# Kernel tuning notes

Measured on AMD Instinct MI355X. Metric: run time of the kernel, lower is better.

## Reference

```python
import jax, jax.numpy as jnp
import numpy as np

QMAX = 127.0          # int8 clip bound (symmetric, preserve-zero)
QDIV = 127.5          # AQT int8 scale divisor: 2**(bits-1) - 0.5


def _safe(s):
    # avoid div-by-zero for all-zero rows/cols
    return jnp.where(s == 0.0, 1.0, s)


def setup_inputs() -> dict:
    key = jax.random.key(0)
    k1, k2 = jax.random.split(key)
    lhs = jax.random.normal(k1, (8192, 4096), dtype=jnp.float32)
    rhs = jax.random.normal(k2, (4096, 4096), dtype=jnp.float32)
    return {"lhs": lhs, "rhs": rhs}


def reference(lhs, rhs):
    # --- dynamic symmetric int8 quantization (AQT abs-max calibration) ---
    # lhs: contract over axis 1 -> per-row scale [M, 1]
    s_l = _safe(jnp.max(jnp.abs(lhs), axis=1, keepdims=True) / QDIV)
    # rhs: contract over axis 0 -> per-column scale [1, N]
    s_r = _safe(jnp.max(jnp.abs(rhs), axis=0, keepdims=True) / QDIV)

    q_l = jnp.clip(jnp.round(lhs / s_l), -QMAX, QMAX).astype(jnp.int8)
    q_r = jnp.clip(jnp.round(rhs / s_r), -QMAX, QMAX).astype(jnp.int8)

    # --- integer matmul with int32 accumulation ---
    acc = jax.lax.dot_general(
        q_l, q_r,
        dimension_numbers=(((1,), (0,)), ((), ())),
        preferred_element_type=jnp.int32,
    )

    # --- dequantize: outer product of per-row / per-column scales ---
    return acc.astype(jnp.float32) * s_l * s_r
```

## Files before the change

kernel.cpp:

```cpp
#include <hip/hip_runtime.h>
#include <stdint.h>

#define M_DIM 8192
#define N_DIM 4096
#define K_DIM 4096
#define QMAXF 127.0f
#define QDIVF 127.5f

typedef int v4i __attribute__((ext_vector_type(4)));

typedef __attribute__((address_space(3))) void lds_void_t;
typedef __attribute__((address_space(1))) const void glb_void_t;

static __device__ __forceinline__ void load_lds16(const void* g, void* l) {
    __builtin_amdgcn_global_load_lds((glb_void_t*)g, (lds_void_t*)l, 16, 0, 0);
}

__global__ __launch_bounds__(256) void prep1_kernel(
        const float* __restrict__ lhs, const float* __restrict__ rhs,
        float* __restrict__ sL, unsigned* __restrict__ bits,
        int8_t* __restrict__ ql) {
    const int t = threadIdx.x;
    if (blockIdx.x < M_DIM) {
        const int row = blockIdx.x;
        const float4* rp = (const float4*)(lhs + (size_t)row * K_DIM);
        float4 v[4];
        float m = 0.0f;
#pragma unroll
        for (int i = 0; i < 4; ++i) {
            v[i] = rp[t + i * 256];
            m = fmaxf(m, fmaxf(fmaxf(fabsf(v[i].x), fabsf(v[i].y)),
                               fmaxf(fabsf(v[i].z), fabsf(v[i].w))));
        }
#pragma unroll
        for (int off = 32; off; off >>= 1) m = fmaxf(m, __shfl_down(m, off, 64));
        __shared__ float wmax[4];
        if ((t & 63) == 0) wmax[t >> 6] = m;
        __syncthreads();
        const float mm = fmaxf(fmaxf(wmax[0], wmax[1]), fmaxf(wmax[2], wmax[3]));
        float s = mm / QDIVF;
        s = (s == 0.0f) ? 1.0f : s;
        if (t == 0) sL[row] = s;
        unsigned* qo = (unsigned*)ql + (size_t)row * 1024;
#pragma unroll
        for (int i = 0; i < 4; ++i) {
            int q0 = (int)fminf(fmaxf(rintf(v[i].x / s), -QMAXF), QMAXF);
            int q1 = (int)fminf(fmaxf(rintf(v[i].y / s), -QMAXF), QMAXF);
            int q2 = (int)fminf(fmaxf(rintf(v[i].z / s), -QMAXF), QMAXF);
            int q3 = (int)fminf(fmaxf(rintf(v[i].w / s), -QMAXF), QMAXF);
            qo[t + i * 256] = (q0 & 255) | ((q1 & 255) << 8) | ((q2 & 255) << 16)
                            | ((unsigned)(q3 & 255) << 24);
        }
    } else {
        const int cb = blockIdx.x - M_DIM;
        const int col = (cb & 15) * 256 + t;
        const int r0 = (cb >> 4) * 64;
        float m = 0.0f;
#pragma unroll 4
        for (int r = 0; r < 64; ++r)
            m = fmaxf(m, fabsf(rhs[(size_t)(r0 + r) * N_DIM + col]));
        atomicMax(&bits[col], __float_as_uint(m));
    }
}

__global__ __launch_bounds__(256) void quant_rhs_t_kernel(
        const float* __restrict__ rhs, const unsigned* __restrict__ bits,
        float* __restrict__ sR, int8_t* __restrict__ qbT) {
    __shared__ __align__(16) int8_t lt[64][80];
    const int n0 = blockIdx.x * 64;
    const int k0 = blockIdx.y * 64;
    const int t = threadIdx.x;
    const int nloc = t & 63;
    const int kq = (t >> 6) * 16;
    float s = __uint_as_float(bits[n0 + nloc]) / QDIVF;
    s = (s == 0.0f) ? 1.0f : s;
    if (blockIdx.y == 0 && t < 64) {
        float ss = __uint_as_float(bits[n0 + t]) / QDIVF;
        sR[n0 + t] = (ss == 0.0f) ? 1.0f : ss;
    }
#pragma unroll
    for (int i = 0; i < 4; ++i) {
        unsigned pack = 0;
#pragma unroll
        for (int j = 0; j < 4; ++j) {
            int kk = kq + i * 4 + j;
            float x = rhs[(size_t)(k0 + kk) * N_DIM + n0 + nloc];
            int q = (int)fminf(fmaxf(rintf(x / s), -QMAXF), QMAXF);
            pack |= (unsigned)(q & 255) << (8 * j);
        }
        *(unsigned*)&lt[nloc][kq + i * 4] = pack;
    }
    __syncthreads();
    const int nn = t >> 2, ch = t & 3;
    v4i val = *(const v4i*)&lt[nn][ch * 16];
    *(v4i*)&qbT[(size_t)(n0 + nn) * K_DIM + k0 + ch * 16] = val;
}


#define BAR() do { asm volatile("" ::: "memory");          \
                   __builtin_amdgcn_s_barrier();           \
                   asm volatile("" ::: "memory"); } while (0)

#define VMCNT(N) asm volatile("s_waitcnt vmcnt(%0)" :: "n"(N) : "memory")

#define TILE(KT, BUF, PAR, SA, SB, VM) do {                                     \
    if (SA) {                                                                   \
        _Pragma("unroll") for (int mm = 0; mm < 4; ++mm)                        \
            an[(PAR) ^ 1][mm] = *(const v4i*)(pa[mm] + ((KT) + 1) * 64);        \
    }                                                                           \
    if (SB) {                                                                   \
        load_lds16(gB0 + (size_t)((KT) + 2) * 64,                               \
                   lds + (((KT) + 2) & 3) * 16384 + sdst);                      \
        load_lds16(gB0 + (size_t)128 * K_DIM + (size_t)((KT) + 2) * 64,         \
                   lds + (((KT) + 2) & 3) * 16384 + 8192 + sdst);               \
    }                                                                           \
    _Pragma("unroll") for (int nn = 0; nn < 8; ++nn)                            \
        bf[nn] = *(const v4i*)(lds + (BUF) * 16384 + boff[nn]);                 \
    __builtin_amdgcn_s_setprio(1);                                              \
    _Pragma("unroll") for (int mm = 0; mm < 4; ++mm)                            \
    _Pragma("unroll") for (int nn = 0; nn < 8; ++nn)                            \
        acc[mm][nn] = __builtin_amdgcn_mfma_i32_16x16x64_i8(                    \
            an[PAR][mm], bf[nn], acc[mm][nn], 0, 0, 0);                         \
    __builtin_amdgcn_s_setprio(0);                                              \
    VMCNT(VM);                                                                  \
    BAR();                                                                      \
} while (0)

__global__ __launch_bounds__(512, 2) void gemm_i8_kernel(
        const int8_t* __restrict__ qa, const int8_t* __restrict__ qbT,
        const float* __restrict__ sL, const float* __restrict__ sR,
        float* __restrict__ out) {
    __shared__ __align__(16) int8_t lds[65536];

    const int t = threadIdx.x;
    const int wave = t >> 6;
    const int lane = t & 63;

    const int bid = blockIdx.x;
    const int xcd = bid & 7;
    const int idx = bid >> 3;
    const int mt = (xcd >> 1) * 8 + (idx >> 3);
    const int nt = (xcd & 1) * 8 + (idx & 7);
    const int brow = mt * 256;
    const int bcol = nt * 256;

    const int wm = (wave >> 1) * 64;
    const int wn = (wave & 1) * 128;

    const int8_t* pa[4];
#pragma unroll
    for (int m = 0; m < 4; ++m)
        pa[m] = qa + (size_t)(brow + wm + m * 16 + (lane & 15)) * K_DIM
                   + (lane >> 4) * 16;

    int boff[8];
#pragma unroll
    for (int n = 0; n < 8; ++n) {
        int row = wn + n * 16 + (lane & 15);
        boff[n] = row * 64 + (((lane >> 4) ^ ((row >> 1) & 3)) * 16);
    }

    v4i acc[4][8];
#pragma unroll
    for (int m = 0; m < 4; ++m)
#pragma unroll
        for (int n = 0; n < 8; ++n) acc[m][n] = (v4i){0, 0, 0, 0};

    const int srow = t >> 2;
    const int lcA = (t & 3) ^ ((srow >> 1) & 3);
    const int8_t* gB0 = qbT + (size_t)(bcol + srow) * K_DIM + lcA * 16;
    const int sdst = t * 16;

    v4i an[2][4], bf[8];

    load_lds16(gB0,                             lds + sdst);
    load_lds16(gB0 + (size_t)128 * K_DIM,       lds + 8192 + sdst);
    load_lds16(gB0 + 64,                        lds + 16384 + sdst);
    load_lds16(gB0 + (size_t)128 * K_DIM + 64,  lds + 16384 + 8192 + sdst);
#pragma unroll
    for (int mm = 0; mm < 4; ++mm) an[0][mm] = *(const v4i*)(pa[mm]);
    VMCNT(6);
    BAR();

    for (int kt = 0; kt < 60; kt += 4) {
        TILE(kt + 0, 0, 0, 1, 1, 6);
        TILE(kt + 1, 1, 1, 1, 1, 6);
        TILE(kt + 2, 2, 0, 1, 1, 6);
        TILE(kt + 3, 3, 1, 1, 1, 6);
    }
    TILE(60, 0, 0, 1, 1, 6);
    TILE(61, 1, 1, 1, 1, 6);
    TILE(62, 2, 0, 1, 0, 4);
    TILE(63, 3, 1, 0, 0, 0);

    const int r4 = (lane >> 4) * 4;
    const int cc = lane & 15;
#pragma unroll
    for (int m = 0; m < 4; ++m) {
        const int grow0 = brow + wm + m * 16 + r4;
        const float s0 = sL[grow0 + 0];
        const float s1 = sL[grow0 + 1];
        const float s2 = sL[grow0 + 2];
        const float s3 = sL[grow0 + 3];
#pragma unroll
        for (int n = 0; n < 8; ++n) {
            const int gcol = bcol + wn + n * 16 + cc;
            const float sc = sR[gcol];
            float* o = out + (size_t)grow0 * N_DIM + gcol;
            o[0 * N_DIM] = (float)acc[m][n][0] * s0 * sc;
            o[1 * N_DIM] = (float)acc[m][n][1] * s1 * sc;
            o[2 * N_DIM] = (float)acc[m][n][2] * s2 * sc;
            o[3 * N_DIM] = (float)acc[m][n][3] * s3 * sc;
        }
    }
}

extern "C" void kernel_launch(void* const* d_in, const int* in_sizes, int n_in,
                              void* d_out, int out_size, void* d_ws, size_t ws_size,
                              hipStream_t stream) {
    const float* lhs = (const float*)d_in[0];
    const float* rhs = (const float*)d_in[1];
    float* out = (float*)d_out;

    uint8_t* ws = (uint8_t*)d_ws;
    int8_t* ql    = (int8_t*)ws;
    int8_t* qbT   = (int8_t*)(ws + 33554432);
    float* sL     = (float*)(ws + 50331648);
    float* sR     = (float*)(ws + 50331648 + 32768);
    unsigned* bits = (unsigned*)(ws + 50331648 + 32768 + 16384);

    hipMemsetAsync(bits, 0, N_DIM * sizeof(unsigned), stream);

    prep1_kernel<<<M_DIM + 1024, 256, 0, stream>>>(lhs, rhs, sL, bits, ql);
    quant_rhs_t_kernel<<<dim3(N_DIM / 64, K_DIM / 64), 256, 0, stream>>>(
        rhs, bits, sR, qbT);
    gemm_i8_kernel<<<dim3((M_DIM / 256) * (N_DIM / 256)), 512, 0, stream>>>(
        ql, qbT, sL, sR, out);
}
```

Before: 263.1 us.

## Stage A tiles through LDS with 4-deep pipeline and 128x128 per-wave tiles

```diff
diff --git a/kernel.cpp b/kernel.cpp
--- a/kernel.cpp
+++ b/kernel.cpp
@@ -103,34 +103,39 @@
 
 #define VMCNT(N) asm volatile("s_waitcnt vmcnt(%0)" :: "n"(N) : "memory")
 
-#define TILE(KT, BUF, PAR, SA, SB, VM) do {                                     \
-    if (SA) {                                                                   \
-        _Pragma("unroll") for (int mm = 0; mm < 4; ++mm)                        \
-            an[(PAR) ^ 1][mm] = *(const v4i*)(pa[mm] + ((KT) + 1) * 64);        \
+#define STAGE_ALL(KT, BQ) do {                                                  \
+    _Pragma("unroll") for (int h = 0; h < 4; ++h)                               \
+        load_lds16(gA0 + (size_t)(h * 64) * K_DIM + (size_t)(KT) * 64,          \
+                   lds + (BQ) * 32768 + h * 4096 + sdst);                       \
+    _Pragma("unroll") for (int h = 0; h < 4; ++h)                               \
+        load_lds16(gB0 + (size_t)(h * 64) * K_DIM + (size_t)(KT) * 64,          \
+                   lds + (BQ) * 32768 + 16384 + h * 4096 + sdst);               \
+} while (0)
+
+#define TILE(KT, P, RDN, S, VM, DOBAR) do {                                     \
+    if (DOBAR) { VMCNT(VM); BAR(); }                                            \
+    if (RDN) {                                                                  \
+        _Pragma("unroll") for (int mm = 0; mm < 8; ++mm)                        \
+            af[(P) ^ 1][mm] = *(const v4i*)(                                    \
+                lds + (((KT) + 1) & 3) * 32768 + aoff[mm]);                     \
+        _Pragma("unroll") for (int nn = 0; nn < 8; ++nn)                        \
+            bf[(P) ^ 1][nn] = *(const v4i*)(                                    \
+                lds + (((KT) + 1) & 3) * 32768 + boff[nn]);                     \
     }                                                                           \
-    if (SB) {                                                                   \
-        load_lds16(gB0 + (size_t)((KT) + 2) * 64,                               \
-                   lds + (((KT) + 2) & 3) * 16384 + sdst);                      \
-        load_lds16(gB0 + (size_t)128 * K_DIM + (size_t)((KT) + 2) * 64,         \
-                   lds + (((KT) + 2) & 3) * 16384 + 8192 + sdst);               \
-    }                                                                           \
-    _Pragma("unroll") for (int nn = 0; nn < 8; ++nn)                            \
-        bf[nn] = *(const v4i*)(lds + (BUF) * 16384 + boff[nn]);                 \
+    if (S) STAGE_ALL((KT) + 3, ((KT) + 3) & 3);                                 \
     __builtin_amdgcn_s_setprio(1);                                              \
-    _Pragma("unroll") for (int mm = 0; mm < 4; ++mm)                            \
+    _Pragma("unroll") for (int mm = 0; mm < 8; ++mm)                            \
     _Pragma("unroll") for (int nn = 0; nn < 8; ++nn)                            \
         acc[mm][nn] = __builtin_amdgcn_mfma_i32_16x16x64_i8(                    \
-            an[PAR][mm], bf[nn], acc[mm][nn], 0, 0, 0);                         \
+            af[P][mm], bf[P][nn], acc[mm][nn], 0, 0, 0);                        \
     __builtin_amdgcn_s_setprio(0);                                              \
-    VMCNT(VM);                                                                  \
-    BAR();                                                                      \
 } while (0)
 
-__global__ __launch_bounds__(512, 2) void gemm_i8_kernel(
+__global__ __launch_bounds__(256, 1) void gemm_i8_kernel(
         const int8_t* __restrict__ qa, const int8_t* __restrict__ qbT,
         const float* __restrict__ sL, const float* __restrict__ sR,
         float* __restrict__ out) {
-    __shared__ __align__(16) int8_t lds[65536];
+    __shared__ __align__(16) int8_t lds[131072];
 
     const int t = threadIdx.x;
     const int wave = t >> 6;
@@ -139,64 +144,67 @@
     const int bid = blockIdx.x;
     const int xcd = bid & 7;
     const int idx = bid >> 3;
-    const int mt = (xcd >> 1) * 8 + (idx >> 3);
-    const int nt = (xcd & 1) * 8 + (idx & 7);
+    const int mt = (xcd >> 1) * 8 + (idx & 7);
+    const int nt = (xcd & 1) * 8 + (idx >> 3);
     const int brow = mt * 256;
     const int bcol = nt * 256;
 
-    const int wm = (wave >> 1) * 64;
+    const int wm = (wave >> 1) * 128;
     const int wn = (wave & 1) * 128;
 
-    const int8_t* pa[4];
-#pragma unroll
-    for (int m = 0; m < 4; ++m)
-        pa[m] = qa + (size_t)(brow + wm + m * 16 + (lane & 15)) * K_DIM
-                   + (lane >> 4) * 16;
-
-    int boff[8];
+    int aoff[8], boff[8];
+#pragma unroll
+    for (int m = 0; m < 8; ++m) {
+        int row = wm + m * 16 + (lane & 15);
+        aoff[m] = row * 64 + (((lane >> 4) ^ ((row >> 1) & 3)) * 16);
+    }
 #pragma unroll
     for (int n = 0; n < 8; ++n) {
         int row = wn + n * 16 + (lane & 15);
-        boff[n] = row * 64 + (((lane >> 4) ^ ((row >> 1) & 3)) * 16);
-    }
-
-    v4i acc[4][8];
-#pragma unroll
-    for (int m = 0; m < 4; ++m)
+        boff[n] = 16384 + row * 64 + (((lane >> 4) ^ ((row >> 1) & 3)) * 16);
+    }
+
+    v4i acc[8][8];
+#pragma unroll
+    for (int m = 0; m < 8; ++m)
 #pragma unroll
         for (int n = 0; n < 8; ++n) acc[m][n] = (v4i){0, 0, 0, 0};
 
     const int srow = t >> 2;
     const int lcA = (t & 3) ^ ((srow >> 1) & 3);
+    const int8_t* gA0 = qa  + (size_t)(brow + srow) * K_DIM + lcA * 16;
     const int8_t* gB0 = qbT + (size_t)(bcol + srow) * K_DIM + lcA * 16;
     const int sdst = t * 16;
 
-    v4i an[2][4], bf[8];
-
-    load_lds16(gB0,                             lds + sdst);
-    load_lds16(gB0 + (size_t)128 * K_DIM,       lds + 8192 + sdst);
-    load_lds16(gB0 + 64,                        lds + 16384 + sdst);
-    load_lds16(gB0 + (size_t)128 * K_DIM + 64,  lds + 16384 + 8192 + sdst);
-#pragma unroll
-    for (int mm = 0; mm < 4; ++mm) an[0][mm] = *(const v4i*)(pa[mm]);
-    VMCNT(6);
+    v4i af[2][8], bf[2][8];
+
+    STAGE_ALL(0, 0);
+    STAGE_ALL(1, 1);
+    STAGE_ALL(2, 2);
+    VMCNT(16);
     BAR();
+#pragma unroll
+    for (int mm = 0; mm < 8; ++mm)
+        af[0][mm] = *(const v4i*)(lds + aoff[mm]);
+#pragma unroll
+    for (int nn = 0; nn < 8; ++nn)
+        bf[0][nn] = *(const v4i*)(lds + boff[nn]);
 
     for (int kt = 0; kt < 60; kt += 4) {
-        TILE(kt + 0, 0, 0, 1, 1, 6);
-        TILE(kt + 1, 1, 1, 1, 1, 6);
-        TILE(kt + 2, 2, 0, 1, 1, 6);
-        TILE(kt + 3, 3, 1, 1, 1, 6);
-    }
-    TILE(60, 0, 0, 1, 1, 6);
-    TILE(61, 1, 1, 1, 1, 6);
-    TILE(62, 2, 0, 1, 0, 4);
-    TILE(63, 3, 1, 0, 0, 0);
+        TILE(kt + 0, 0, 1, 1, 8, 1);
+        TILE(kt + 1, 1, 1, 1, 8, 1);
+        TILE(kt + 2, 0, 1, 1, 8, 1);
+        TILE(kt + 3, 1, 1, 1, 8, 1);
+    }
+    TILE(60, 0, 1, 1, 8, 1);
+    TILE(61, 1, 1, 0, 8, 1);
+    TILE(62, 0, 1, 0, 0, 1);
+    TILE(63, 1, 0, 0, 0, 0);
 
     const int r4 = (lane >> 4) * 4;
     const int cc = lane & 15;
 #pragma unroll
-    for (int m = 0; m < 4; ++m) {
+    for (int m = 0; m < 8; ++m) {
         const int grow0 = brow + wm + m * 16 + r4;
         const float s0 = sL[grow0 + 0];
         const float s1 = sL[grow0 + 1];
@@ -234,6 +242,6 @@
     prep1_kernel<<<M_DIM + 1024, 256, 0, stream>>>(lhs, rhs, sL, bits, ql);
     quant_rhs_t_kernel<<<dim3(N_DIM / 64, K_DIM / 64), 256, 0, stream>>>(
         rhs, bits, sR, qbT);
-    gemm_i8_kernel<<<dim3((M_DIM / 256) * (N_DIM / 256)), 512, 0, stream>>>(
+    gemm_i8_kernel<<<dim3((M_DIM / 256) * (N_DIM / 256)), 256, 0, stream>>>(
         ql, qbT, sL, sR, out);
 }
```

Result: faster. 224.7 us (-14.6%).
